# Performance work log

Hardware: AMD Instinct MI355X
Metric: run time of the kernel (lower is better)

## Reference

```python
import jax, jax.numpy as jnp
import numpy as np

B, T, D_MODEL = 2, 2048, 1024
H, D_HEAD, R = 16, 64, 16
CAUSAL = True


def setup_inputs() -> dict:
    key = jax.random.key(0)
    ks = jax.random.split(key, 6)
    return {
        "x": jax.random.normal(ks[0], (B, T, D_MODEL), dtype=jnp.float32),
        "W_qkv": jax.random.normal(ks[1], (D_MODEL, 3 * D_MODEL), dtype=jnp.float32) * 0.02,
        "W_q_lsr": jax.random.normal(ks[2], (H, D_HEAD, R), dtype=jnp.float32) * 0.1,
        "W_k_lsr": jax.random.normal(ks[3], (H, D_HEAD, R), dtype=jnp.float32) * 0.1,
        "core": jax.random.normal(ks[4], (H, R), dtype=jnp.float32),
        "W_o": jax.random.normal(ks[5], (D_MODEL, D_MODEL), dtype=jnp.float32) * 0.02,
    }


def reference(x, W_qkv, W_q_lsr, W_k_lsr, core, W_o):
    Bx, Tx, D = x.shape
    Hh, Dh, Rr = W_q_lsr.shape
    # Fused QKV projection, then split heads -> (B, H, T, D_head)
    qkv = x @ W_qkv  # (B, T, 3D)
    q, k, v = jnp.split(qkv, 3, axis=-1)
    q = q.reshape(Bx, Tx, Hh, Dh).transpose(0, 2, 1, 3)
    k = k.reshape(Bx, Tx, Hh, Dh).transpose(0, 2, 1, 3)
    v = v.reshape(Bx, Tx, Hh, Dh).transpose(0, 2, 1, 3)
    # Low-rank (LSR) projections of q and k; core + 1/sqrt(R) scaling on q side
    scale = 1.0 / jnp.sqrt(jnp.asarray(max(Rr, 1), dtype=jnp.float32))
    q_lr = jnp.einsum('bhtd,hdr->bhtr', q, W_q_lsr) * core[None, :, None, :] * scale
    k_lr = jnp.einsum('bhtd,hdr->bhtr', k, W_k_lsr)
    # Low-rank scores (B, H, T, T)
    scores = jnp.einsum('bhir,bhjr->bhij', q_lr, k_lr)
    if CAUSAL:
        mask = jnp.tril(jnp.ones((Tx, Tx), dtype=bool))
        scores = jnp.where(mask[None, None], scores, -jnp.inf)
    attn = jax.nn.softmax(scores, axis=-1)
    out = jnp.einsum('bhij,bhjd->bhid', attn, v)  # (B, H, T, D_head)
    out = out.transpose(0, 2, 1, 3).reshape(Bx, Tx, D)
    return out @ W_o
```

## Files before the change

### kernel.cpp

```cpp
#include <hip/hip_runtime.h>
#include <hip/hip_bf16.h>

#define BB 2
#define TT 2048
#define DD 1024
#define HH 16
#define DH 64
#define RR 16
#define BT (BB*TT)
#define BH (BB*HH)
#define D3 (3*DD)
#define NC 1536

typedef __bf16 bf16x8 __attribute__((ext_vector_type(8)));
typedef __bf16 bf16x4 __attribute__((ext_vector_type(4)));
typedef float f32x4 __attribute__((ext_vector_type(4)));
typedef short short4v __attribute__((ext_vector_type(4)));

__device__ __forceinline__ float bf2f(unsigned short u) {
  unsigned int v = ((unsigned int)u) << 16;
  return __builtin_bit_cast(float, v);
}
__device__ __forceinline__ unsigned short f2bf(float f) {
  unsigned int x = __builtin_bit_cast(unsigned int, f);
  unsigned int r = x + 0x7fffu + ((x >> 16) & 1u);
  return (unsigned short)(r >> 16);
}
__device__ __forceinline__ short4v pack_bf16x4(float a, float b, float c, float d) {
  uint2 u;
  u.x = (unsigned)f2bf(a) | ((unsigned)f2bf(b) << 16);
  u.y = (unsigned)f2bf(c) | ((unsigned)f2bf(d) << 16);
  return __builtin_bit_cast(short4v, u);
}
__device__ __forceinline__ short4v pack4_cvt(float a, float b, float c, float d) {
  bf16x4 v = {(__bf16)a, (__bf16)b, (__bf16)c, (__bf16)d};
  return __builtin_bit_cast(short4v, v);
}

#define NEG_BIG (-1e30f)

__device__ __forceinline__ void async_copy16(const void* g, void* l) {
  __builtin_amdgcn_global_load_lds((const __attribute__((address_space(1))) void*)g,
                                   (__attribute__((address_space(3))) void*)l, 16, 0, 0);
}

__global__ __launch_bounds__(256) void prep_fused(const float* __restrict__ x,
                                                  const float* __restrict__ Wqkv,
                                                  const float* __restrict__ Wql,
                                                  const float* __restrict__ Wkl,
                                                  const float* __restrict__ core,
                                                  const float* __restrict__ Wo,
                                                  unsigned short* __restrict__ x_bf,
                                                  unsigned short* __restrict__ Wcomb_t,
                                                  unsigned short* __restrict__ Wo_t) {
  __shared__ float tile[32][33];
  __shared__ float Aq[64][65], Ak[64][65], Lq[64][16], Lk[64][16], cs[16];
  const int bid = blockIdx.x, tid = threadIdx.x;
  if (bid < 2048) {
    int i = (bid * 256 + tid) * 8;
    float4 a = *(const float4*)&x[i];
    float4 b = *(const float4*)&x[i + 4];
    unsigned short t[8] = {f2bf(a.x), f2bf(a.y), f2bf(a.z), f2bf(a.w),
                           f2bf(b.x), f2bf(b.y), f2bf(b.z), f2bf(b.w)};
    *(uint4*)&x_bf[i] = *(const uint4*)t;
  } else if (bid < 4096) {
    const float* in; unsigned short* out; int C, coff, lb;
    if (bid < 3072) { in = Wo;   out = Wo_t;    C = DD; coff = 0;    lb = bid - 2048; }
    else            { in = Wqkv; out = Wcomb_t; C = D3; coff = 2048; lb = bid - 3072; }
    const int tx = tid & 31, ty = tid >> 5;
    const int bx = lb & 31, by = lb >> 5;
    const int xx = bx * 32 + tx, y0 = by * 32;
#pragma unroll
    for (int i = 0; i < 32; i += 8)
      tile[ty + i][tx] = in[(size_t)(y0 + ty + i) * C + coff + xx];
    __syncthreads();
    const int xo = y0 + tx, yo0 = bx * 32;
#pragma unroll
    for (int i = 0; i < 32; i += 8)
      out[(size_t)(yo0 + ty + i) * DD + xo] = f2bf(tile[tx][ty + i]);
  } else {
    const int l = bid - 4096;
    const int d0 = (l & 15) * 64, h = l >> 4;
#pragma unroll
    for (int p = 0; p < 16; p++) {
      int idx = p * 256 + tid, dd = idx >> 6, e = idx & 63;
      Aq[dd][e] = Wqkv[(size_t)(d0 + dd) * D3 + h * 64 + e];
      Ak[dd][e] = Wqkv[(size_t)(d0 + dd) * D3 + DD + h * 64 + e];
    }
#pragma unroll
    for (int p = 0; p < 4; p++) {
      int idx = p * 256 + tid, e = idx >> 4, r = idx & 15;
      Lq[e][r] = Wql[h * 1024 + e * 16 + r];
      Lk[e][r] = Wkl[h * 1024 + e * 16 + r];
    }
    if (tid < 16) cs[tid] = core[h * 16 + tid];
    __syncthreads();
    const int dd = tid & 63, rg = tid >> 6;
    float aq[4] = {}, ak[4] = {};
    for (int e = 0; e < 64; e++) {
      float xq = Aq[dd][e], xk = Ak[dd][e];
#pragma unroll
      for (int j = 0; j < 4; j++) {
        aq[j] += xq * Lq[e][rg * 4 + j];
        ak[j] += xk * Lk[e][rg * 4 + j];
      }
    }
#pragma unroll
    for (int j = 0; j < 4; j++) {
      int r = rg * 4 + j;
      Wcomb_t[(size_t)(1024 + h * 16 + r) * DD + d0 + dd] =
          f2bf(aq[j] * cs[r] * (0.25f * 1.4426950408889634f));
      Wcomb_t[(size_t)(1280 + h * 16 + r) * DD + d0 + dd] = f2bf(ak[j]);
    }
  }
}

__device__ __forceinline__ void gemm64_core(const unsigned short* __restrict__ A,
                                            const unsigned short* __restrict__ Bt,
                                            int K, int bm, int bn,
                                            int tid, int g, int c, int wm, int wn,
                                            f32x4 acc[2][4]) {
  __shared__ __attribute__((aligned(16))) unsigned short As[2][2 * 2048];
  __shared__ __attribute__((aligned(16))) unsigned short Bs[2][2 * 4096];
  const int e0 = tid * 8;
  const int r0 = e0 >> 5, q0 = e0 & 31;
  const unsigned short* Ar  = &A[(size_t)(bm * 64 + r0) * K + q0];
  const unsigned short* Br0 = &Bt[(size_t)(bn * 128 + r0) * K + q0];
  const unsigned short* Br1 = &Bt[(size_t)(bn * 128 + 64 + r0) * K + q0];
  async_copy16(Ar,       &As[0][e0]);
  async_copy16(Ar  + 32, &As[0][2048 + e0]);
  async_copy16(Br0,      &Bs[0][e0]);
  async_copy16(Br1,      &Bs[0][2048 + e0]);
  async_copy16(Br0 + 32, &Bs[0][4096 + e0]);
  async_copy16(Br1 + 32, &Bs[0][4096 + 2048 + e0]);
  __syncthreads();
  const int nsteps = K >> 6;
  for (int t = 0; t < nsteps; t++) {
    const int cur = t & 1, nxt = cur ^ 1;
    if (t + 1 < nsteps) {
      const int k1 = (t + 1) << 6;
      async_copy16(Ar  + k1,      &As[nxt][e0]);
      async_copy16(Ar  + k1 + 32, &As[nxt][2048 + e0]);
      async_copy16(Br0 + k1,      &Bs[nxt][e0]);
      async_copy16(Br1 + k1,      &Bs[nxt][2048 + e0]);
      async_copy16(Br0 + k1 + 32, &Bs[nxt][4096 + e0]);
      async_copy16(Br1 + k1 + 32, &Bs[nxt][4096 + 2048 + e0]);
    }
#pragma unroll
    for (int p = 0; p < 2; p++) {
      bf16x8 af[2];
#pragma unroll
      for (int mt = 0; mt < 2; mt++)
        af[mt] = *(const bf16x8*)&As[cur][p * 2048 + (wm * 32 + mt * 16 + c) * 32 + g * 8];
#pragma unroll
      for (int nt = 0; nt < 4; nt++) {
        bf16x8 bf = *(const bf16x8*)&Bs[cur][p * 4096 + (wn * 64 + nt * 16 + c) * 32 + g * 8];
#pragma unroll
        for (int mt = 0; mt < 2; mt++)
          acc[mt][nt] = __builtin_amdgcn_mfma_f32_16x16x32_bf16(af[mt], bf, acc[mt][nt], 0, 0, 0);
      }
    }
    __syncthreads();
  }
}

__global__ __launch_bounds__(256) void gemm64_f32(const unsigned short* __restrict__ A,
                                                  const unsigned short* __restrict__ Bt,
                                                  float* __restrict__ C,
                                                  int M, int N, int K) {
  const int tid = threadIdx.x, lane = tid & 63;
  const int g = lane >> 4, c = lane & 15;
  const int wid = tid >> 6, wm = wid >> 1, wn = wid & 1;
  const int bm = blockIdx.y, bn = blockIdx.x;
  f32x4 acc[2][4] = {};
  gemm64_core(A, Bt, K, bm, bn, tid, g, c, wm, wn, acc);
#pragma unroll
  for (int mt = 0; mt < 2; mt++)
#pragma unroll
    for (int nt = 0; nt < 4; nt++)
#pragma unroll
      for (int r = 0; r < 4; r++) {
        int row = bm * 64 + wm * 32 + mt * 16 + g * 4 + r;
        int col = bn * 128 + wn * 64 + nt * 16 + c;
        C[(size_t)row * N + col] = acc[mt][nt][r];
      }
}

__global__ __launch_bounds__(256) void gemm_fused(const unsigned short* __restrict__ A,
                                                  const unsigned short* __restrict__ Bt,
                                                  unsigned short* __restrict__ qls,
                                                  unsigned short* __restrict__ klr,
                                                  unsigned short* __restrict__ vt,
                                                  int M, int N, int K) {
  const int tid = threadIdx.x, lane = tid & 63;
  const int g = lane >> 4, c = lane & 15;
  const int wid = tid >> 6, wm = wid >> 1, wn = wid & 1;
  const int bm = blockIdx.y, bn = blockIdx.x;
  f32x4 acc[2][4] = {};
  gemm64_core(A, Bt, K, bm, bn, tid, g, c, wm, wn, acc);
#pragma unroll
  for (int mt = 0; mt < 2; mt++)
#pragma unroll
    for (int nt = 0; nt < 4; nt++) {
      int colb = bn * 128 + wn * 64 + nt * 16;
      int tg0 = bm * 64 + wm * 32 + mt * 16 + g * 4;
      int b = tg0 >> 11, t0 = tg0 & 2047;
      if (colb < 1024) {
        int h = colb >> 6, d = (colb & 63) + c;
        uint2 pk = __builtin_bit_cast(uint2, pack_bf16x4(acc[mt][nt][0], acc[mt][nt][1],
                                                         acc[mt][nt][2], acc[mt][nt][3]));
        size_t idx = (size_t)(b * 16 + h) * (TT / 4) * 256 + (size_t)(t0 >> 2) * 256 + d * 4;
        *(uint2*)&vt[idx] = pk;
      } else if (colb < 1280) {
        int h = (colb - 1024) >> 4;
        size_t base = (size_t)(b * 16 + h) * TT;
#pragma unroll
        for (int r = 0; r < 4; r++)
          qls[(base + t0 + r) * 16 + c] = f2bf(acc[mt][nt][r]);
      } else {
        int h = (colb - 1280) >> 4;
        size_t base = (size_t)(b * 16 + h) * TT;
#pragma unroll
        for (int r = 0; r < 4; r++)
          klr[(base + t0 + r) * 16 + c] = f2bf(acc[mt][nt][r]);
      }
    }
}

__global__ __launch_bounds__(256, 3) void flash_lsr(const unsigned short* __restrict__ qls,
                                                    const unsigned short* __restrict__ klr,
                                                    const unsigned short* __restrict__ vt,
                                                    unsigned short* __restrict__ attn) {
  const int bh = blockIdx.x & 31, b = bh >> 4, h = bh & 15;
  const int qt = 31 - (blockIdx.x >> 5);
  const int tid = threadIdx.x, lane = tid & 63, w = tid >> 6;
  const int g = lane >> 4, c = lane & 15;
  const int q0 = qt * 64, jmax = qt >> 1;

  __shared__ __attribute__((aligned(16))) unsigned short Ks[2][128 * 20];

  const size_t qbase = (size_t)bh * TT;
  const short4v qf = __builtin_bit_cast(short4v,
      *(const uint2*)&qls[(qbase + q0 + w * 16 + c) * 16 + g * 4]);
  const int qg = q0 + w * 16 + c;
  float mi = NEG_BIG, li = 0.f;
  f32x4 oa[4] = {};
  const f32x4 zero = {0.f, 0.f, 0.f, 0.f};
  const size_t kb = (size_t)bh * TT * 16;
  const size_t vb = (size_t)bh * TT * 64;

  uint4 kr = *(const uint4*)&klr[kb + tid * 8];

  int p = 0;
  f32x4 s[8];
  for (int jt = 0; jt <= jmax; jt++) {
    *(uint4*)&Ks[p][(tid >> 1) * 20 + (tid & 1) * 8] = kr;
    __syncthreads();
    if (jt < jmax)
      kr = *(const uint4*)&klr[kb + (size_t)(jt + 1) * 2048 + tid * 8];
    const unsigned short* Kb = Ks[p];
#pragma unroll
    for (int nt = 0; nt < 8; nt++) {
      short4v kf = __builtin_bit_cast(short4v, *(const uint2*)&Kb[(nt * 16 + c) * 20 + g * 4]);
      s[nt] = __builtin_amdgcn_mfma_f32_16x16x16bf16_1k(kf, qf, zero, 0, 0, 0);
    }
    if (jt == jmax) {
#pragma unroll
      for (int nt = 0; nt < 8; nt++)
#pragma unroll
        for (int r = 0; r < 4; r++) {
          int jg = jt * 128 + nt * 16 + g * 4 + r;
          if (jg > qg) s[nt][r] = NEG_BIG;
        }
    }
    f32x4 vm = s[0];
#pragma unroll
    for (int nt = 1; nt < 8; nt++)
#pragma unroll
      for (int r = 0; r < 4; r++) vm[r] = fmaxf(vm[r], s[nt][r]);
    float rm = fmaxf(fmaxf(vm[0], vm[1]), fmaxf(vm[2], vm[3]));
    rm = fmaxf(rm, __shfl_xor(rm, 16, 64));
    rm = fmaxf(rm, __shfl_xor(rm, 32, 64));
    float mnew = fmaxf(mi, rm);
    float alpha = __builtin_amdgcn_exp2f(mi - mnew);
    mi = mnew;
    f32x4 vs = zero;
#pragma unroll
    for (int nt = 0; nt < 8; nt++)
#pragma unroll
      for (int r = 0; r < 4; r++) {
        float pv = __builtin_amdgcn_exp2f(s[nt][r] - mnew);
        s[nt][r] = pv;
        vs[r] += pv;
      }
    float rs = (vs[0] + vs[1]) + (vs[2] + vs[3]);
    rs += __shfl_xor(rs, 16, 64);
    rs += __shfl_xor(rs, 32, 64);
    li = li * alpha + rs;
#pragma unroll
    for (int nd = 0; nd < 4; nd++)
#pragma unroll
      for (int r = 0; r < 4; r++) oa[nd][r] *= alpha;
    const unsigned short* vp = &vt[vb + (size_t)jt * 8192];
#pragma unroll
    for (int kc = 0; kc < 8; kc++) {
      short4v pf = pack4_cvt(s[kc][0], s[kc][1], s[kc][2], s[kc][3]);
#pragma unroll
      for (int nd = 0; nd < 4; nd++) {
        uint2 vv = *(const uint2*)&vp[(kc * 4 + g) * 256 + (nd * 16 + c) * 4];
        short4v vf = __builtin_bit_cast(short4v, vv);
        oa[nd] = __builtin_amdgcn_mfma_f32_16x16x16bf16_1k(vf, pf, oa[nd], 0, 0, 0);
      }
    }
    p ^= 1;
  }

  const float inv = 1.f / li;
  const size_t rowb = ((size_t)b * TT + q0 + w * 16 + c) * DD + h * 64;
#pragma unroll
  for (int nd = 0; nd < 4; nd++) {
    short4v pk = pack4_cvt(oa[nd][0] * inv, oa[nd][1] * inv,
                           oa[nd][2] * inv, oa[nd][3] * inv);
    *(uint2*)&attn[rowb + nd * 16 + g * 4] = __builtin_bit_cast(uint2, pk);
  }
}

extern "C" void kernel_launch(void* const* d_in, const int* in_sizes, int n_in,
                              void* d_out, int out_size, void* d_ws, size_t ws_size,
                              hipStream_t stream) {
  const float* x      = (const float*)d_in[0];
  const float* W_qkv  = (const float*)d_in[1];
  const float* W_qlsr = (const float*)d_in[2];
  const float* W_klsr = (const float*)d_in[3];
  const float* core   = (const float*)d_in[4];
  const float* W_o    = (const float*)d_in[5];
  float* out = (float*)d_out;

  char* ws = (char*)d_ws;
  unsigned short* x_bf    = (unsigned short*)ws; ws += (size_t)BT * DD * 2;
  unsigned short* Wcomb_t = (unsigned short*)ws; ws += (size_t)NC * DD * 2;
  unsigned short* Wo_t    = (unsigned short*)ws; ws += (size_t)DD * DD * 2;
  unsigned short* qls     = (unsigned short*)ws; ws += (size_t)BH * TT * 16 * 2;
  unsigned short* klr     = (unsigned short*)ws; ws += (size_t)BH * TT * 16 * 2;
  unsigned short* vt      = (unsigned short*)ws; ws += (size_t)BH * TT * 64 * 2;
  unsigned short* attn    = (unsigned short*)ws; ws += (size_t)BT * DD * 2;

  prep_fused<<<4352, 256, 0, stream>>>(x, W_qkv, W_qlsr, W_klsr, core, W_o,
                                       x_bf, Wcomb_t, Wo_t);
  gemm_fused<<<dim3(NC / 128, BT / 64), 256, 0, stream>>>(x_bf, Wcomb_t, qls, klr, vt, BT, NC, DD);
  flash_lsr<<<dim3(32 * BH), 256, 0, stream>>>(qls, klr, vt, attn);
  gemm64_f32<<<dim3(DD / 128, BT / 64), 256, 0, stream>>>(attn, Wo_t, out, BT, DD, DD);
}
```

Measured before the change: 174.6 us.

## Process two 64-row query tiles per flash block to reuse K/V loads

Each flash attention block now handles 128 query rows, split into two independent 64-row sub-tiles, instead of 64. Each K tile staged in shared memory and each V fragment loaded from global memory then feeds two sets of MFMAs, halving K/V traffic per query. In exchange the grid is halved to 512 blocks, launch bounds drop to 2 blocks per SM, and register pressure doubles. The causal last tile is also processed at 128-key granularity for both halves, so some masked work is wasted.

Result: faster. 165.4 us (-5.2%).

```diff
diff --git a/kernel.cpp b/kernel.cpp
--- a/kernel.cpp
+++ b/kernel.cpp
@@ -227,24 +227,26 @@
     }
 }
 
-__global__ __launch_bounds__(256, 3) void flash_lsr(const unsigned short* __restrict__ qls,
+__global__ __launch_bounds__(256, 2) void flash_lsr(const unsigned short* __restrict__ qls,
                                                     const unsigned short* __restrict__ klr,
                                                     const unsigned short* __restrict__ vt,
                                                     unsigned short* __restrict__ attn) {
   const int bh = blockIdx.x & 31, b = bh >> 4, h = bh & 15;
-  const int qt = 31 - (blockIdx.x >> 5);
+  const int qt = 15 - (blockIdx.x >> 5);
   const int tid = threadIdx.x, lane = tid & 63, w = tid >> 6;
   const int g = lane >> 4, c = lane & 15;
-  const int q0 = qt * 64, jmax = qt >> 1;
+  const int q0 = qt * 128, jmax = qt;
 
   __shared__ __attribute__((aligned(16))) unsigned short Ks[2][128 * 20];
 
   const size_t qbase = (size_t)bh * TT;
-  const short4v qf = __builtin_bit_cast(short4v,
+  const short4v qfA = __builtin_bit_cast(short4v,
       *(const uint2*)&qls[(qbase + q0 + w * 16 + c) * 16 + g * 4]);
-  const int qg = q0 + w * 16 + c;
-  float mi = NEG_BIG, li = 0.f;
-  f32x4 oa[4] = {};
+  const short4v qfB = __builtin_bit_cast(short4v,
+      *(const uint2*)&qls[(qbase + q0 + 64 + w * 16 + c) * 16 + g * 4]);
+  const int qgA = q0 + w * 16 + c, qgB = qgA + 64;
+  float miA = NEG_BIG, liA = 0.f, miB = NEG_BIG, liB = 0.f;
+  f32x4 oaA[4] = {}, oaB[4] = {};
   const f32x4 zero = {0.f, 0.f, 0.f, 0.f};
   const size_t kb = (size_t)bh * TT * 16;
   const size_t vb = (size_t)bh * TT * 64;
@@ -252,7 +254,7 @@
   uint4 kr = *(const uint4*)&klr[kb + tid * 8];
 
   int p = 0;
-  f32x4 s[8];
+  f32x4 sA[8], sB[8];
   for (int jt = 0; jt <= jmax; jt++) {
     *(uint4*)&Ks[p][(tid >> 1) * 20 + (tid & 1) * 8] = kr;
     __syncthreads();
@@ -262,7 +264,8 @@
 #pragma unroll
     for (int nt = 0; nt < 8; nt++) {
       short4v kf = __builtin_bit_cast(short4v, *(const uint2*)&Kb[(nt * 16 + c) * 20 + g * 4]);
-      s[nt] = __builtin_amdgcn_mfma_f32_16x16x16bf16_1k(kf, qf, zero, 0, 0, 0);
+      sA[nt] = __builtin_amdgcn_mfma_f32_16x16x16bf16_1k(kf, qfA, zero, 0, 0, 0);
+      sB[nt] = __builtin_amdgcn_mfma_f32_16x16x16bf16_1k(kf, qfB, zero, 0, 0, 0);
     }
     if (jt == jmax) {
 #pragma unroll
@@ -270,58 +273,69 @@
 #pragma unroll
         for (int r = 0; r < 4; r++) {
           int jg = jt * 128 + nt * 16 + g * 4 + r;
-          if (jg > qg) s[nt][r] = NEG_BIG;
+          if (jg > qgA) sA[nt][r] = NEG_BIG;
+          if (jg > qgB) sB[nt][r] = NEG_BIG;
         }
     }
-    f32x4 vm = s[0];
-#pragma unroll
-    for (int nt = 1; nt < 8; nt++)
-#pragma unroll
-      for (int r = 0; r < 4; r++) vm[r] = fmaxf(vm[r], s[nt][r]);
-    float rm = fmaxf(fmaxf(vm[0], vm[1]), fmaxf(vm[2], vm[3]));
-    rm = fmaxf(rm, __shfl_xor(rm, 16, 64));
-    rm = fmaxf(rm, __shfl_xor(rm, 32, 64));
-    float mnew = fmaxf(mi, rm);
-    float alpha = __builtin_amdgcn_exp2f(mi - mnew);
-    mi = mnew;
-    f32x4 vs = zero;
-#pragma unroll
-    for (int nt = 0; nt < 8; nt++)
-#pragma unroll
-      for (int r = 0; r < 4; r++) {
-        float pv = __builtin_amdgcn_exp2f(s[nt][r] - mnew);
-        s[nt][r] = pv;
-        vs[r] += pv;
-      }
-    float rs = (vs[0] + vs[1]) + (vs[2] + vs[3]);
-    rs += __shfl_xor(rs, 16, 64);
-    rs += __shfl_xor(rs, 32, 64);
-    li = li * alpha + rs;
-#pragma unroll
-    for (int nd = 0; nd < 4; nd++)
-#pragma unroll
-      for (int r = 0; r < 4; r++) oa[nd][r] *= alpha;
+    auto softmax = [&](f32x4 (&s)[8], float& mi, float& li, f32x4 (&oa)[4]) {
+      f32x4 vm = s[0];
+#pragma unroll
+      for (int nt = 1; nt < 8; nt++)
+#pragma unroll
+        for (int r = 0; r < 4; r++) vm[r] = fmaxf(vm[r], s[nt][r]);
+      float rm = fmaxf(fmaxf(vm[0], vm[1]), fmaxf(vm[2], vm[3]));
+      rm = fmaxf(rm, __shfl_xor(rm, 16, 64));
+      rm = fmaxf(rm, __shfl_xor(rm, 32, 64));
+      float mnew = fmaxf(mi, rm);
+      float alpha = __builtin_amdgcn_exp2f(mi - mnew);
+      mi = mnew;
+      f32x4 vs = zero;
+#pragma unroll
+      for (int nt = 0; nt < 8; nt++)
+#pragma unroll
+        for (int r = 0; r < 4; r++) {
+          float pv = __builtin_amdgcn_exp2f(s[nt][r] - mnew);
+          s[nt][r] = pv;
+          vs[r] += pv;
+        }
+      float rs = (vs[0] + vs[1]) + (vs[2] + vs[3]);
+      rs += __shfl_xor(rs, 16, 64);
+      rs += __shfl_xor(rs, 32, 64);
+      li = li * alpha + rs;
+#pragma unroll
+      for (int nd = 0; nd < 4; nd++)
+#pragma unroll
+        for (int r = 0; r < 4; r++) oa[nd][r] *= alpha;
+    };
+    softmax(sA, miA, liA, oaA);
+    softmax(sB, miB, liB, oaB);
     const unsigned short* vp = &vt[vb + (size_t)jt * 8192];
 #pragma unroll
     for (int kc = 0; kc < 8; kc++) {
-      short4v pf = pack4_cvt(s[kc][0], s[kc][1], s[kc][2], s[kc][3]);
+      short4v pfA = pack4_cvt(sA[kc][0], sA[kc][1], sA[kc][2], sA[kc][3]);
+      short4v pfB = pack4_cvt(sB[kc][0], sB[kc][1], sB[kc][2], sB[kc][3]);
 #pragma unroll
       for (int nd = 0; nd < 4; nd++) {
         uint2 vv = *(const uint2*)&vp[(kc * 4 + g) * 256 + (nd * 16 + c) * 4];
         short4v vf = __builtin_bit_cast(short4v, vv);
-        oa[nd] = __builtin_amdgcn_mfma_f32_16x16x16bf16_1k(vf, pf, oa[nd], 0, 0, 0);
+        oaA[nd] = __builtin_amdgcn_mfma_f32_16x16x16bf16_1k(vf, pfA, oaA[nd], 0, 0, 0);
+        oaB[nd] = __builtin_amdgcn_mfma_f32_16x16x16bf16_1k(vf, pfB, oaB[nd], 0, 0, 0);
       }
     }
     p ^= 1;
   }
 
-  const float inv = 1.f / li;
-  const size_t rowb = ((size_t)b * TT + q0 + w * 16 + c) * DD + h * 64;
+  const float invA = 1.f / liA, invB = 1.f / liB;
+  const size_t rowA = ((size_t)b * TT + q0 + w * 16 + c) * DD + h * 64;
+  const size_t rowB = rowA + (size_t)64 * DD;
 #pragma unroll
   for (int nd = 0; nd < 4; nd++) {
-    short4v pk = pack4_cvt(oa[nd][0] * inv, oa[nd][1] * inv,
-                           oa[nd][2] * inv, oa[nd][3] * inv);
-    *(uint2*)&attn[rowb + nd * 16 + g * 4] = __builtin_bit_cast(uint2, pk);
+    short4v pkA = pack4_cvt(oaA[nd][0] * invA, oaA[nd][1] * invA,
+                            oaA[nd][2] * invA, oaA[nd][3] * invA);
+    *(uint2*)&attn[rowA + nd * 16 + g * 4] = __builtin_bit_cast(uint2, pkA);
+    short4v pkB = pack4_cvt(oaB[nd][0] * invB, oaB[nd][1] * invB,
+                            oaB[nd][2] * invB, oaB[nd][3] * invB);
+    *(uint2*)&attn[rowB + nd * 16 + g * 4] = __builtin_bit_cast(uint2, pkB);
   }
 }
 
@@ -348,6 +362,6 @@
   prep_fused<<<4352, 256, 0, stream>>>(x, W_qkv, W_qlsr, W_klsr, core, W_o,
                                        x_bf, Wcomb_t, Wo_t);
   gemm_fused<<<dim3(NC / 128, BT / 64), 256, 0, stream>>>(x_bf, Wcomb_t, qls, klr, vt, BT, NC, DD);
-  flash_lsr<<<dim3(32 * BH), 256, 0, stream>>>(qls, klr, vt, attn);
+  flash_lsr<<<dim3(16 * BH), 256, 0, stream>>>(qls, klr, vt, attn);
   gemm64_f32<<<dim3(DD / 128, BT / 64), 256, 0, stream>>>(attn, Wo_t, out, BT, DD, DD);
 }
```

## Pair long and short causal query tiles per block to balance attention work

Applied to the files above, without the earlier changes.

Each flash-attention block now processes two query tiles, a long one (31-z) and a short one (z), sharing the K tile loads and V fragment reads across both during the overlapping key range. This balances causal work across blocks and halves the grid from 1024 to 512 blocks, while reusing loaded K and V data. In exchange, register use roughly doubles for accumulators, so launch bounds drop from 3 to 2 waves-per-SIMD occupancy, and fewer blocks may underfill the GPU.

Result: slower. 197.7 us (+13.2%).

```diff
diff --git a/kernel.cpp b/kernel.cpp
--- a/kernel.cpp
+++ b/kernel.cpp
@@ -227,52 +227,35 @@
     }
 }
 
-__global__ __launch_bounds__(256, 3) void flash_lsr(const unsigned short* __restrict__ qls,
+__global__ __launch_bounds__(256, 2) void flash_lsr(const unsigned short* __restrict__ qls,
                                                     const unsigned short* __restrict__ klr,
                                                     const unsigned short* __restrict__ vt,
                                                     unsigned short* __restrict__ attn) {
   const int bh = blockIdx.x & 31, b = bh >> 4, h = bh & 15;
-  const int qt = 31 - (blockIdx.x >> 5);
+  const int z = blockIdx.x >> 5;
   const int tid = threadIdx.x, lane = tid & 63, w = tid >> 6;
   const int g = lane >> 4, c = lane & 15;
-  const int q0 = qt * 64, jmax = qt >> 1;
+  const int q0L = (31 - z) * 64, q0S = z * 64;
+  const int jmaxL = (31 - z) >> 1, jmaxS = z >> 1;
 
   __shared__ __attribute__((aligned(16))) unsigned short Ks[2][128 * 20];
 
   const size_t qbase = (size_t)bh * TT;
-  const short4v qf = __builtin_bit_cast(short4v,
-      *(const uint2*)&qls[(qbase + q0 + w * 16 + c) * 16 + g * 4]);
-  const int qg = q0 + w * 16 + c;
-  float mi = NEG_BIG, li = 0.f;
-  f32x4 oa[4] = {};
+  const short4v qfL = __builtin_bit_cast(short4v,
+      *(const uint2*)&qls[(qbase + q0L + w * 16 + c) * 16 + g * 4]);
+  const short4v qfS = __builtin_bit_cast(short4v,
+      *(const uint2*)&qls[(qbase + q0S + w * 16 + c) * 16 + g * 4]);
+  const int qgL = q0L + w * 16 + c, qgS = q0S + w * 16 + c;
+  float miL = NEG_BIG, liL = 0.f, miS = NEG_BIG, liS = 0.f;
+  f32x4 oaL[4] = {}, oaS[4] = {};
   const f32x4 zero = {0.f, 0.f, 0.f, 0.f};
   const size_t kb = (size_t)bh * TT * 16;
   const size_t vb = (size_t)bh * TT * 64;
 
   uint4 kr = *(const uint4*)&klr[kb + tid * 8];
 
-  int p = 0;
-  f32x4 s[8];
-  for (int jt = 0; jt <= jmax; jt++) {
-    *(uint4*)&Ks[p][(tid >> 1) * 20 + (tid & 1) * 8] = kr;
-    __syncthreads();
-    if (jt < jmax)
-      kr = *(const uint4*)&klr[kb + (size_t)(jt + 1) * 2048 + tid * 8];
-    const unsigned short* Kb = Ks[p];
-#pragma unroll
-    for (int nt = 0; nt < 8; nt++) {
-      short4v kf = __builtin_bit_cast(short4v, *(const uint2*)&Kb[(nt * 16 + c) * 20 + g * 4]);
-      s[nt] = __builtin_amdgcn_mfma_f32_16x16x16bf16_1k(kf, qf, zero, 0, 0, 0);
-    }
-    if (jt == jmax) {
-#pragma unroll
-      for (int nt = 0; nt < 8; nt++)
-#pragma unroll
-        for (int r = 0; r < 4; r++) {
-          int jg = jt * 128 + nt * 16 + g * 4 + r;
-          if (jg > qg) s[nt][r] = NEG_BIG;
-        }
-    }
+  f32x4 sL[8], sS[8];
+  auto smax = [&](f32x4 (&s)[8], float& mi, float& li, f32x4 (&oa)[4]) {
     f32x4 vm = s[0];
 #pragma unroll
     for (int nt = 1; nt < 8; nt++)
@@ -301,27 +284,93 @@
     for (int nd = 0; nd < 4; nd++)
 #pragma unroll
       for (int r = 0; r < 4; r++) oa[nd][r] *= alpha;
+  };
+
+  int p = 0, jt = 0;
+  for (; jt <= jmaxS; jt++) {
+    *(uint4*)&Ks[p][(tid >> 1) * 20 + (tid & 1) * 8] = kr;
+    __syncthreads();
+    if (jt < jmaxL)
+      kr = *(const uint4*)&klr[kb + (size_t)(jt + 1) * 2048 + tid * 8];
+    const unsigned short* Kb = Ks[p];
+#pragma unroll
+    for (int nt = 0; nt < 8; nt++) {
+      short4v kf = __builtin_bit_cast(short4v, *(const uint2*)&Kb[(nt * 16 + c) * 20 + g * 4]);
+      sL[nt] = __builtin_amdgcn_mfma_f32_16x16x16bf16_1k(kf, qfL, zero, 0, 0, 0);
+      sS[nt] = __builtin_amdgcn_mfma_f32_16x16x16bf16_1k(kf, qfS, zero, 0, 0, 0);
+    }
+    if (jt == jmaxS) {
+#pragma unroll
+      for (int nt = 0; nt < 8; nt++)
+#pragma unroll
+        for (int r = 0; r < 4; r++) {
+          int jg = jt * 128 + nt * 16 + g * 4 + r;
+          if (jg > qgS) sS[nt][r] = NEG_BIG;
+        }
+    }
+    smax(sL, miL, liL, oaL);
+    smax(sS, miS, liS, oaS);
     const unsigned short* vp = &vt[vb + (size_t)jt * 8192];
 #pragma unroll
     for (int kc = 0; kc < 8; kc++) {
-      short4v pf = pack4_cvt(s[kc][0], s[kc][1], s[kc][2], s[kc][3]);
+      short4v pfL = pack4_cvt(sL[kc][0], sL[kc][1], sL[kc][2], sL[kc][3]);
+      short4v pfS = pack4_cvt(sS[kc][0], sS[kc][1], sS[kc][2], sS[kc][3]);
 #pragma unroll
       for (int nd = 0; nd < 4; nd++) {
         uint2 vv = *(const uint2*)&vp[(kc * 4 + g) * 256 + (nd * 16 + c) * 4];
         short4v vf = __builtin_bit_cast(short4v, vv);
-        oa[nd] = __builtin_amdgcn_mfma_f32_16x16x16bf16_1k(vf, pf, oa[nd], 0, 0, 0);
+        oaL[nd] = __builtin_amdgcn_mfma_f32_16x16x16bf16_1k(vf, pfL, oaL[nd], 0, 0, 0);
+        oaS[nd] = __builtin_amdgcn_mfma_f32_16x16x16bf16_1k(vf, pfS, oaS[nd], 0, 0, 0);
       }
     }
     p ^= 1;
   }
-
-  const float inv = 1.f / li;
-  const size_t rowb = ((size_t)b * TT + q0 + w * 16 + c) * DD + h * 64;
+  for (; jt <= jmaxL; jt++) {
+    *(uint4*)&Ks[p][(tid >> 1) * 20 + (tid & 1) * 8] = kr;
+    __syncthreads();
+    if (jt < jmaxL)
+      kr = *(const uint4*)&klr[kb + (size_t)(jt + 1) * 2048 + tid * 8];
+    const unsigned short* Kb = Ks[p];
+#pragma unroll
+    for (int nt = 0; nt < 8; nt++) {
+      short4v kf = __builtin_bit_cast(short4v, *(const uint2*)&Kb[(nt * 16 + c) * 20 + g * 4]);
+      sL[nt] = __builtin_amdgcn_mfma_f32_16x16x16bf16_1k(kf, qfL, zero, 0, 0, 0);
+    }
+    if (jt == jmaxL) {
+#pragma unroll
+      for (int nt = 0; nt < 8; nt++)
+#pragma unroll
+        for (int r = 0; r < 4; r++) {
+          int jg = jt * 128 + nt * 16 + g * 4 + r;
+          if (jg > qgL) sL[nt][r] = NEG_BIG;
+        }
+    }
+    smax(sL, miL, liL, oaL);
+    const unsigned short* vp = &vt[vb + (size_t)jt * 8192];
+#pragma unroll
+    for (int kc = 0; kc < 8; kc++) {
+      short4v pfL = pack4_cvt(sL[kc][0], sL[kc][1], sL[kc][2], sL[kc][3]);
+#pragma unroll
+      for (int nd = 0; nd < 4; nd++) {
+        uint2 vv = *(const uint2*)&vp[(kc * 4 + g) * 256 + (nd * 16 + c) * 4];
+        short4v vf = __builtin_bit_cast(short4v, vv);
+        oaL[nd] = __builtin_amdgcn_mfma_f32_16x16x16bf16_1k(vf, pfL, oaL[nd], 0, 0, 0);
+      }
+    }
+    p ^= 1;
+  }
+
+  const float invL = 1.f / liL, invS = 1.f / liS;
+  const size_t rowL = ((size_t)b * TT + q0L + w * 16 + c) * DD + h * 64;
+  const size_t rowS = ((size_t)b * TT + q0S + w * 16 + c) * DD + h * 64;
 #pragma unroll
   for (int nd = 0; nd < 4; nd++) {
-    short4v pk = pack4_cvt(oa[nd][0] * inv, oa[nd][1] * inv,
-                           oa[nd][2] * inv, oa[nd][3] * inv);
-    *(uint2*)&attn[rowb + nd * 16 + g * 4] = __builtin_bit_cast(uint2, pk);
+    short4v pkL = pack4_cvt(oaL[nd][0] * invL, oaL[nd][1] * invL,
+                            oaL[nd][2] * invL, oaL[nd][3] * invL);
+    *(uint2*)&attn[rowL + nd * 16 + g * 4] = __builtin_bit_cast(uint2, pkL);
+    short4v pkS = pack4_cvt(oaS[nd][0] * invS, oaS[nd][1] * invS,
+                            oaS[nd][2] * invS, oaS[nd][3] * invS);
+    *(uint2*)&attn[rowS + nd * 16 + g * 4] = __builtin_bit_cast(uint2, pkS);
   }
 }
 
@@ -348,6 +397,6 @@
   prep_fused<<<4352, 256, 0, stream>>>(x, W_qkv, W_qlsr, W_klsr, core, W_o,
                                        x_bf, Wcomb_t, Wo_t);
   gemm_fused<<<dim3(NC / 128, BT / 64), 256, 0, stream>>>(x_bf, Wcomb_t, qls, klr, vt, BT, NC, DD);
-  flash_lsr<<<dim3(32 * BH), 256, 0, stream>>>(qls, klr, vt, attn);
+  flash_lsr<<<dim3(16 * BH), 256, 0, stream>>>(qls, klr, vt, attn);
   gemm64_f32<<<dim3(DD / 128, BT / 64), 256, 0, stream>>>(attn, Wo_t, out, BT, DD, DD);
 }
```
